# Kernel tuning notes

Hardware: AMD Instinct MI355X
Metric: run time of the kernel (lower is better)

The kernel has to match this reference:

```python
import jax, jax.numpy as jnp
import numpy as np

H, HKV, D, HID = 16, 8, 128, 2048   # heads, kv heads, head_dim, hidden
TOTAL, NSEG = 2048, 4               # packed tokens, number of sequences
SEG = TOTAL // NSEG
EPS = 1e-6


def setup_inputs() -> dict:
    key = jax.random.key(0)
    ks = jax.random.split(key, 8)
    x = jax.random.normal(ks[0], (1, TOTAL, HID), jnp.float32)
    # RoPE tables, positions restart at each packed segment
    inv_freq = 1.0 / (10000.0 ** (jnp.arange(0, D, 2, dtype=jnp.float32) / D))
    pos = jnp.tile(jnp.arange(SEG, dtype=jnp.float32), NSEG)  # [TOTAL]
    ang = pos[:, None] * inv_freq[None, :]                    # [TOTAL, D/2]
    emb = jnp.concatenate([ang, ang], axis=-1)                # [TOTAL, D]
    cos, sin = jnp.cos(emb), jnp.sin(emb)
    std = 0.02
    Wq = jax.random.normal(ks[1], (H * D, HID), jnp.float32) * std
    Wk = jax.random.normal(ks[2], (HKV * D, HID), jnp.float32) * std
    Wv = jax.random.normal(ks[3], (HKV * D, HID), jnp.float32) * std
    Wo = jax.random.normal(ks[4], (HID, H * D), jnp.float32) * std
    q_norm_w = jnp.ones((D,), jnp.float32)
    k_norm_w = jnp.ones((D,), jnp.float32)
    cu_seqlens = (jnp.arange(NSEG + 1, dtype=jnp.int32) * SEG)
    return {
        'x': x, 'cos': cos, 'sin': sin,
        'cu_seqlens': cu_seqlens, 'max_seqlen': SEG,
        'Wq': Wq, 'Wk': Wk, 'Wv': Wv, 'Wo': Wo,
        'q_norm_w': q_norm_w, 'k_norm_w': k_norm_w,
    }


def _rms(x, w):
    xf = x.astype(jnp.float32)
    var = jnp.mean(xf * xf, axis=-1, keepdims=True)
    return (w * xf * jax.lax.rsqrt(var + EPS)).astype(x.dtype)


def _rotate_half(x):
    x1, x2 = jnp.split(x, 2, axis=-1)
    return jnp.concatenate([-x2, x1], axis=-1)


def reference(x, cos, sin, cu_seqlens, max_seqlen, Wq, Wk, Wv, Wo, q_norm_w, k_norm_w):
    total = x.shape[1]
    xt = x[0]                                   # [total, HID]
    q = (xt @ Wq.T).reshape(total, H, D)
    k = (xt @ Wk.T).reshape(total, HKV, D)
    v = (xt @ Wv.T).reshape(total, HKV, D)
    q = _rms(q, q_norm_w)
    k = _rms(k, k_norm_w)
    c = cos[:, None, :]                          # [total, 1, D]
    s = sin[:, None, :]
    q = q * c + _rotate_half(q) * s
    k = k * c + _rotate_half(k) * s
    # GQA: repeat kv heads
    n_rep = H // HKV
    k = jnp.repeat(k, n_rep, axis=1)             # [total, H, D]
    v = jnp.repeat(v, n_rep, axis=1)
    # varlen causal mask (block-diagonal causal from cu_seqlens)
    idx = jnp.arange(total)
    seg = jnp.searchsorted(cu_seqlens[1:], idx, side='right')
    mask = (seg[:, None] == seg[None, :]) & (idx[:, None] >= idx[None, :])
    scale = 1.0 / jnp.sqrt(jnp.float32(D))
    scores = jnp.einsum('qhd,khd->hqk', q, k) * scale
    scores = jnp.where(mask[None, :, :], scores, -jnp.inf)
    probs = jax.nn.softmax(scores, axis=-1)
    out = jnp.einsum('hqk,khd->qhd', probs, v).reshape(1, total, H * D)
    return out @ Wo.T
```

## Files before the change

kernel.cpp:

```cpp
#include <hip/hip_runtime.h>
#include <hip/hip_bf16.h>
#include <stdint.h>

#define TOTAL 2048
#define NSEG  4
#define SEG   512
#define NH    16
#define NKV   8
#define DH    128
#define HID   2048
#define QKV_N 4096

typedef __attribute__((ext_vector_type(8))) __bf16 bf16x8;
typedef __attribute__((ext_vector_type(8))) unsigned short u16x8;
typedef __attribute__((ext_vector_type(4))) float f32x4;

__device__ __forceinline__ unsigned short f2bf(float f) {
  unsigned int u = __float_as_uint(f);
  u += 0x7fffu + ((u >> 16) & 1u);
  return (unsigned short)(u >> 16);
}

__device__ __forceinline__ void gll16(const void* g, void* l) {
  __builtin_amdgcn_global_load_lds(
      (const __attribute__((address_space(1))) void*)(uintptr_t)g,
      (__attribute__((address_space(3))) void*)(uint32_t)(uintptr_t)l,
      16, 0, 0);
}
__device__ __forceinline__ void cfence() { asm volatile("" ::: "memory"); }

__global__ __launch_bounds__(256) void cvt_all(const float* __restrict__ x,
                                               const float* __restrict__ wq,
                                               const float* __restrict__ wk,
                                               const float* __restrict__ wv,
                                               const float* __restrict__ wo,
                                               unsigned short* __restrict__ xb,
                                               unsigned short* __restrict__ wqkvb,
                                               unsigned short* __restrict__ wob) {
  const int N0 = 1048576, N1 = 1048576, N2 = 524288, N3 = 524288;
  int i = blockIdx.x * 256 + threadIdx.x;
  #pragma unroll
  for (int it = 0; it < 4; ++it, i += 1048576) {
    const float* src; unsigned short* dst; int j = i;
    if (j < N0)              { src = x;  dst = xb; }
    else if ((j -= N0) < N1) { src = wq; dst = wqkvb; }
    else if ((j -= N1) < N2) { src = wk; dst = wqkvb + 4194304; }
    else if ((j -= N2) < N3) { src = wv; dst = wqkvb + 6291456; }
    else                     { j -= N3; src = wo; dst = wob; }
    float4 v = reinterpret_cast<const float4*>(src)[j];
    ushort4 o;
    o.x = f2bf(v.x); o.y = f2bf(v.y); o.z = f2bf(v.z); o.w = f2bf(v.w);
    reinterpret_cast<ushort4*>(dst)[j] = o;
  }
}

template<int BM>
__global__ __launch_bounds__(BM == 128 ? 256 : 128)
void gemm_bt(const unsigned short* __restrict__ A,
             const unsigned short* __restrict__ B,
             float* __restrict__ C, int M, int N, int K) {
  constexpr int NW  = (BM == 128) ? 4 : 2;
  constexpr int APW = (BM / 8) / NW;
  constexpr int BPW = 16 / NW;
  __shared__ unsigned short As[2][BM * 64];
  __shared__ unsigned short Bs[2][128 * 64];
  const int t    = threadIdx.x;
  const int lane = t & 63;
  const int w    = t >> 6;
  const int wr   = (BM == 128) ? (w >> 1) * 64 : 0;
  const int wc   = (BM == 128) ? (w & 1) * 64 : w * 64;
  const long row0 = (long)blockIdx.y * BM;
  const long col0 = (long)blockIdx.x * 128;

  const int lrow  = lane >> 3;
  const int gslot = (lane & 7) ^ (lrow & 7);
  const unsigned short* gA[APW]; int lA[APW];
  const unsigned short* gB[BPW]; int lB[BPW];
  #pragma unroll
  for (int j = 0; j < APW; ++j) {
    const int c = w * APW + j;
    gA[j] = A + (row0 + c * 8 + lrow) * (long)K + gslot * 8;
    lA[j] = c * 512;
  }
  #pragma unroll
  for (int j = 0; j < BPW; ++j) {
    const int c = w * BPW + j;
    gB[j] = B + (col0 + c * 8 + lrow) * (long)K + gslot * 8;
    lB[j] = c * 512;
  }

  const int fr = lane & 15;
  const int l4 = lane >> 4;

  f32x4 acc[4][4];
  #pragma unroll
  for (int m = 0; m < 4; ++m)
    #pragma unroll
    for (int n = 0; n < 4; ++n) acc[m][n] = (f32x4){0.f, 0.f, 0.f, 0.f};

  #pragma unroll
  for (int j = 0; j < APW; ++j) gll16(gA[j], &As[0][lA[j]]);
  #pragma unroll
  for (int j = 0; j < BPW; ++j) gll16(gB[j], &Bs[0][lB[j]]);
  asm volatile("s_waitcnt vmcnt(0)" ::: "memory");
  __builtin_amdgcn_s_barrier();
  cfence();

  int cur = 0;
  for (int k0 = 0; k0 < K; k0 += 64) {
    if (k0 + 64 < K) {
      #pragma unroll
      for (int j = 0; j < APW; ++j) gll16(gA[j] + k0 + 64, &As[cur ^ 1][lA[j]]);
      #pragma unroll
      for (int j = 0; j < BPW; ++j) gll16(gB[j] + k0 + 64, &Bs[cur ^ 1][lB[j]]);
      if constexpr (BM == 128) asm volatile("s_waitcnt vmcnt(8)" ::: "memory");
      else                     asm volatile("s_waitcnt vmcnt(12)" ::: "memory");
    } else {
      asm volatile("s_waitcnt vmcnt(0)" ::: "memory");
    }
    __builtin_amdgcn_s_barrier();
    cfence();

    #pragma unroll
    for (int kk = 0; kk < 2; ++kk) {
      bf16x8 af[4], bfv[4];
      #pragma unroll
      for (int m = 0; m < 4; ++m) {
        const int ra = wr + m * 16 + fr;
        af[m] = *reinterpret_cast<const bf16x8*>(
            &As[cur][ra * 64 + (((kk * 4 + l4) ^ (ra & 7)) * 8)]);
      }
      #pragma unroll
      for (int n = 0; n < 4; ++n) {
        const int rb = wc + n * 16 + fr;
        bfv[n] = *reinterpret_cast<const bf16x8*>(
            &Bs[cur][rb * 64 + (((kk * 4 + l4) ^ (rb & 7)) * 8)]);
      }
      #pragma unroll
      for (int m = 0; m < 4; ++m)
        #pragma unroll
        for (int n = 0; n < 4; ++n)
          acc[m][n] = __builtin_amdgcn_mfma_f32_16x16x32_bf16(af[m], bfv[n], acc[m][n], 0, 0, 0);
    }

    cfence();
    __builtin_amdgcn_s_barrier();
    cfence();
    cur ^= 1;
  }

  const int crow = (lane >> 4) * 4;
  const int ccol = lane & 15;
  #pragma unroll
  for (int m = 0; m < 4; ++m)
    #pragma unroll
    for (int n = 0; n < 4; ++n)
      #pragma unroll
      for (int r = 0; r < 4; ++r)
        C[(row0 + wr + m * 16 + crow + r) * (long)N + col0 + wc + n * 16 + ccol] =
            acc[m][n][r];
}

__global__ __launch_bounds__(256) void norm_rope(const float* __restrict__ Cqkv,
                                                 const float* __restrict__ cosb,
                                                 const float* __restrict__ sinb,
                                                 const float* __restrict__ qw,
                                                 const float* __restrict__ kw,
                                                 unsigned short* __restrict__ qb2,
                                                 unsigned short* __restrict__ ktb) {
  const int lane = threadIdx.x & 63;
  const int t  = blockIdx.x * 4 + (threadIdx.x >> 6);
  const int hs = blockIdx.y;

  const float* row = Cqkv + (size_t)t * QKV_N + hs * DH;
  float a = row[lane];
  float b = row[lane + 64];

  float ss = a * a + b * b;
  #pragma unroll
  for (int off = 32; off; off >>= 1) ss += __shfl_xor(ss, off, 64);
  float r = rsqrtf(ss * (1.0f / 128.0f) + 1e-6f);
  const float* wgt = (hs < 16) ? qw : kw;
  a = a * r * wgt[lane];
  b = b * r * wgt[lane + 64];
  float c0 = cosb[t * DH + lane],      c1 = cosb[t * DH + lane + 64];
  float s0 = sinb[t * DH + lane],      s1 = sinb[t * DH + lane + 64];
  float o0 = a * c0 - b * s0;
  float o1 = b * c1 + a * s1;

  unsigned short* dst = (hs < 16)
      ? qb2 + ((size_t)hs * TOTAL + t) * DH
      : ktb + ((size_t)(hs - 16) * TOTAL + t) * DH;
  dst[lane]      = f2bf(o0);
  dst[lane + 64] = f2bf(o1);
}

__global__ __launch_bounds__(256) void vt_kernel(const float* __restrict__ Cqkv,
                                                 unsigned short* __restrict__ vtb) {
  __shared__ unsigned short tile[64][132];
  const int tid = threadIdx.x;
  const int t0  = blockIdx.x * 64;
  const int hkv = blockIdx.y;
  const float* src = Cqkv + (size_t)t0 * QKV_N + (NH + NKV) * DH + hkv * DH;
  #pragma unroll
  for (int it = 0; it < 8; ++it) {
    const int i   = it * 256 + tid;
    const int row = i >> 5;
    const int c4  = i & 31;
    float4 v = *reinterpret_cast<const float4*>(src + (size_t)row * QKV_N + c4 * 4);
    ushort4 o;
    o.x = f2bf(v.x); o.y = f2bf(v.y); o.z = f2bf(v.z); o.w = f2bf(v.w);
    *reinterpret_cast<ushort4*>(&tile[row][c4 * 4]) = o;
  }
  __syncthreads();
  #pragma unroll
  for (int it = 0; it < 4; ++it) {
    const int i  = it * 256 + tid;
    const int d  = i >> 3;
    const int tc = i & 7;
    u16x8 o;
    #pragma unroll
    for (int j = 0; j < 8; ++j) o[j] = tile[tc * 8 + j][d];
    *reinterpret_cast<u16x8*>(vtb + ((size_t)hkv * DH + d) * TOTAL + t0 + tc * 8) = o;
  }
}

__global__ __launch_bounds__(256) void attn_mfma(const unsigned short* __restrict__ qb2,
                                                 const unsigned short* __restrict__ ktb,
                                                 const unsigned short* __restrict__ vtb,
                                                 unsigned short* __restrict__ aob) {
  __shared__ unsigned short Ks[2][64 * 128];
  __shared__ unsigned short Vt[2][128 * 64];
  __shared__ unsigned short ps[4][16][72];

  const int tid  = threadIdx.x;
  const int lane = tid & 63;
  const int w    = tid >> 6;
  const int b    = blockIdx.x;
  const int qt   = 7 - (b & 7);
  const int h    = (b >> 3) & 15;
  const int seg  = b >> 7;
  const int hkv  = h >> 1;
  const int q0   = seg * SEG + qt * 64;
  const int l15  = lane & 15;
  const int l4   = lane >> 4;

  const unsigned short* qptr = qb2 + ((size_t)h * TOTAL + q0 + w * 16 + l15) * DH + l4 * 8;
  bf16x8 aq[4];
  #pragma unroll
  for (int ks = 0; ks < 4; ++ks)
    aq[ks] = *reinterpret_cast<const bf16x8*>(qptr + ks * 32);

  const unsigned short* kbase = ktb + (size_t)hkv * TOTAL * DH;
  const unsigned short* vbase = vtb + (size_t)hkv * DH * TOTAL;

  int ksrc[4], vsrc[4], ldst[4];
  #pragma unroll
  for (int j = 0; j < 4; ++j) {
    const int cc = w * 4 + j;
    const int kr = cc * 4 + (lane >> 4);
    ksrc[j] = kr * DH + (((lane & 15) ^ (kr & 7)) * 8);
    const int vd = cc * 8 + (lane >> 3);
    vsrc[j] = vd * TOTAL + (((lane & 7) ^ (vd & 7)) * 8);
    ldst[j] = cc * 512;
  }

  f32x4 acc[8];
  #pragma unroll
  for (int n = 0; n < 8; ++n) acc[n] = (f32x4){0.f, 0.f, 0.f, 0.f};
  float m_r[4] = {-1e30f, -1e30f, -1e30f, -1e30f};
  float l_r[4] = {0.f, 0.f, 0.f, 0.f};

  const float scale = 0.08838834764831845f;
  const int kvS = seg * SEG;

  #pragma unroll
  for (int j = 0; j < 4; ++j) {
    gll16(kbase + (size_t)kvS * DH + ksrc[j], &Ks[0][ldst[j]]);
    gll16(vbase + kvS + vsrc[j], &Vt[0][ldst[j]]);
  }
  asm volatile("s_waitcnt vmcnt(0)" ::: "memory");
  __builtin_amdgcn_s_barrier();
  cfence();

  int cur = 0;
  for (int kt = 0; kt <= qt; ++kt) {
    const int kv0 = kvS + kt * 64;
    if (kt < qt) {
      #pragma unroll
      for (int j = 0; j < 4; ++j) {
        gll16(kbase + (size_t)(kv0 + 64) * DH + ksrc[j], &Ks[cur ^ 1][ldst[j]]);
        gll16(vbase + (kv0 + 64) + vsrc[j], &Vt[cur ^ 1][ldst[j]]);
      }
      asm volatile("s_waitcnt vmcnt(8)" ::: "memory");
    } else {
      asm volatile("s_waitcnt vmcnt(0)" ::: "memory");
    }
    __builtin_amdgcn_s_barrier();
    cfence();

    const bool diag = (kt == qt);

    f32x4 sv[4];
    #pragma unroll
    for (int c = 0; c < 4; ++c) {
      if (diag && c * 16 > w * 16 + 15) {
        sv[c] = (f32x4){-1e30f, -1e30f, -1e30f, -1e30f};
      } else {
        f32x4 s = (f32x4){0.f, 0.f, 0.f, 0.f};
        const int kr = c * 16 + l15;
        #pragma unroll
        for (int ks = 0; ks < 4; ++ks) {
          const int byte = (kr << 8) + (((ks * 32 + l4 * 8) * 2) ^ ((kr & 7) << 4));
          bf16x8 bk = *reinterpret_cast<const bf16x8*>((const char*)Ks[cur] + byte);
          s = __builtin_amdgcn_mfma_f32_16x16x32_bf16(aq[ks], bk, s, 0, 0, 0);
        }
        sv[c] = s;
      }
    }

    float p[4][4];
    #pragma unroll
    for (int r = 0; r < 4; ++r) {
      const int qq = w * 16 + l4 * 4 + r;
      float mx = -1e30f;
      #pragma unroll
      for (int c = 0; c < 4; ++c) {
        float s = sv[c][r] * scale;
        if (diag) {
          const int kk = c * 16 + l15;
          if (kk > qq) s = -1e30f;
        }
        p[c][r] = s;
        mx = fmaxf(mx, s);
      }
      #pragma unroll
      for (int off = 1; off < 16; off <<= 1) mx = fmaxf(mx, __shfl_xor(mx, off));
      const float nm = fmaxf(m_r[r], mx);
      const float f  = __expf(m_r[r] - nm);
      m_r[r] = nm;
      float ls = 0.f;
      #pragma unroll
      for (int c = 0; c < 4; ++c) { p[c][r] = __expf(p[c][r] - nm); ls += p[c][r]; }
      #pragma unroll
      for (int off = 1; off < 16; off <<= 1) ls += __shfl_xor(ls, off);
      l_r[r] = l_r[r] * f + ls;
      #pragma unroll
      for (int n = 0; n < 8; ++n) acc[n][r] *= f;
    }

    #pragma unroll
    for (int c = 0; c < 4; ++c)
      #pragma unroll
      for (int r = 0; r < 4; ++r)
        ps[w][l4 * 4 + r][c * 16 + l15] = f2bf(p[c][r]);

    #pragma unroll
    for (int ks2 = 0; ks2 < 2; ++ks2) {
      if (diag && ks2 * 32 > w * 16 + 15) continue;
      bf16x8 pa = *reinterpret_cast<const bf16x8*>(&ps[w][l15][ks2 * 32 + l4 * 8]);
      #pragma unroll
      for (int n = 0; n < 8; ++n) {
        const int d = n * 16 + l15;
        const int byte = (d << 7) + (((ks2 * 32 + l4 * 8) * 2) ^ ((d & 7) << 4));
        bf16x8 bv = *reinterpret_cast<const bf16x8*>((const char*)Vt[cur] + byte);
        acc[n] = __builtin_amdgcn_mfma_f32_16x16x32_bf16(pa, bv, acc[n], 0, 0, 0);
      }
    }

    cfence();
    __builtin_amdgcn_s_barrier();
    cfence();
    cur ^= 1;
  }

  #pragma unroll
  for (int r = 0; r < 4; ++r) {
    const float inv = 1.0f / l_r[r];
    unsigned short* orow = aob + ((size_t)(q0 + w * 16 + l4 * 4 + r) * NH + h) * DH;
    #pragma unroll
    for (int n = 0; n < 8; ++n)
      orow[n * 16 + l15] = f2bf(acc[n][r] * inv);
  }
}

extern "C" void kernel_launch(void* const* d_in, const int* in_sizes, int n_in,
                              void* d_out, int out_size, void* d_ws, size_t ws_size,
                              hipStream_t stream) {
  const float* x    = (const float*)d_in[0];
  const float* cosb = (const float*)d_in[1];
  const float* sinb = (const float*)d_in[2];
  const float* Wq   = (const float*)d_in[5];
  const float* Wk   = (const float*)d_in[6];
  const float* Wv   = (const float*)d_in[7];
  const float* Wo   = (const float*)d_in[8];
  const float* qw   = (const float*)d_in[9];
  const float* kw   = (const float*)d_in[10];
  float* out = (float*)d_out;

  char* ws = (char*)d_ws;
  unsigned short* xb    = (unsigned short*)(ws + 0);
  unsigned short* Wqkvb = (unsigned short*)(ws + (8u  << 20));
  unsigned short* Wob   = (unsigned short*)(ws + (24u << 20));
  float*          Cqkv  = (float*)         (ws + (32u << 20));
  unsigned short* qb2   = (unsigned short*)(ws + (64u << 20));
  unsigned short* ktb   = (unsigned short*)(ws + (72u << 20));
  unsigned short* vtb   = (unsigned short*)(ws + (76u << 20));
  unsigned short* aob   = (unsigned short*)(ws + (80u << 20));

  cvt_all<<<4096, 256, 0, stream>>>(x, Wq, Wk, Wv, Wo, xb, Wqkvb, Wob);

  {
    dim3 g(QKV_N / 128, TOTAL / 128);
    gemm_bt<128><<<g, 256, 0, stream>>>(xb, Wqkvb, Cqkv, TOTAL, QKV_N, HID);
  }

  {
    dim3 g(TOTAL / 4, 24);
    norm_rope<<<g, 256, 0, stream>>>(Cqkv, cosb, sinb, qw, kw, qb2, ktb);
  }
  {
    dim3 g(TOTAL / 64, NKV);
    vt_kernel<<<g, 256, 0, stream>>>(Cqkv, vtb);
  }

  attn_mfma<<<NSEG * NH * 8, 256, 0, stream>>>(qb2, ktb, vtb, aob);

  {
    dim3 g(HID / 128, TOTAL / 64);
    gemm_bt<64><<<g, 128, 0, stream>>>(aob, Wob, out, TOTAL, HID, HID);
  }
}
```

Measured before the change: 122.7 us.

## Fuse QK RMSNorm, RoPE and V transpose into QKV GEMM epilogue

Adds a dedicated QKV GEMM kernel whose epilogue computes per-head RMSNorm via cross-wave shared reductions, applies RoPE, and writes bf16 Q/K or transposed V directly. This removes the fp32 QKV intermediate round trip through global memory and two separate kernel launches. The epilogue reuses the 69KB shared buffer for a padded tile, which raises LDS use and may lower occupancy.

```diff
diff --git a/kernel.cpp b/kernel.cpp
--- a/kernel.cpp
+++ b/kernel.cpp
@@ -51,6 +51,176 @@
     ushort4 o;
     o.x = f2bf(v.x); o.y = f2bf(v.y); o.z = f2bf(v.z); o.w = f2bf(v.w);
     reinterpret_cast<ushort4*>(dst)[j] = o;
+  }
+}
+
+__global__ __launch_bounds__(256)
+void gemm_qkv(const unsigned short* __restrict__ A,
+              const unsigned short* __restrict__ B,
+              const float* __restrict__ cosb,
+              const float* __restrict__ sinb,
+              const float* __restrict__ qw,
+              const float* __restrict__ kw,
+              unsigned short* __restrict__ qb2,
+              unsigned short* __restrict__ ktb,
+              unsigned short* __restrict__ vtb) {
+  __shared__ char smem[69120] __attribute__((aligned(16)));
+  unsigned short* As0 = (unsigned short*)smem;
+  unsigned short* Bs0 = (unsigned short*)(smem + 32768);
+  const int K = HID;
+  const int t    = threadIdx.x;
+  const int lane = t & 63;
+  const int w    = t >> 6;
+  const int wr   = (w >> 1) * 64;
+  const int wc   = (w & 1) * 64;
+  const long row0 = (long)blockIdx.y * 128;
+  const long col0 = (long)blockIdx.x * 128;
+
+  const int lrow  = lane >> 3;
+  const int gslot = (lane & 7) ^ (lrow & 7);
+  const unsigned short* gA[4]; const unsigned short* gB[4]; int loff[4];
+  #pragma unroll
+  for (int j = 0; j < 4; ++j) {
+    const int c = w * 4 + j;
+    gA[j] = A + (row0 + c * 8 + lrow) * (long)K + gslot * 8;
+    gB[j] = B + (col0 + c * 8 + lrow) * (long)K + gslot * 8;
+    loff[j] = c * 512;
+  }
+
+  const int fr = lane & 15;
+  const int l4 = lane >> 4;
+
+  f32x4 acc[4][4];
+  #pragma unroll
+  for (int m = 0; m < 4; ++m)
+    #pragma unroll
+    for (int n = 0; n < 4; ++n) acc[m][n] = (f32x4){0.f, 0.f, 0.f, 0.f};
+
+  #pragma unroll
+  for (int j = 0; j < 4; ++j) { gll16(gA[j], As0 + loff[j]); gll16(gB[j], Bs0 + loff[j]); }
+  asm volatile("s_waitcnt vmcnt(0)" ::: "memory");
+  __builtin_amdgcn_s_barrier();
+  cfence();
+
+  int cur = 0;
+  for (int k0 = 0; k0 < K; k0 += 64) {
+    if (k0 + 64 < K) {
+      #pragma unroll
+      for (int j = 0; j < 4; ++j) {
+        gll16(gA[j] + k0 + 64, As0 + (cur ^ 1) * 8192 + loff[j]);
+        gll16(gB[j] + k0 + 64, Bs0 + (cur ^ 1) * 8192 + loff[j]);
+      }
+      asm volatile("s_waitcnt vmcnt(8)" ::: "memory");
+    } else {
+      asm volatile("s_waitcnt vmcnt(0)" ::: "memory");
+    }
+    __builtin_amdgcn_s_barrier();
+    cfence();
+
+    #pragma unroll
+    for (int kk = 0; kk < 2; ++kk) {
+      bf16x8 af[4], bfv[4];
+      #pragma unroll
+      for (int m = 0; m < 4; ++m) {
+        const int ra = wr + m * 16 + fr;
+        af[m] = *reinterpret_cast<const bf16x8*>(
+            As0 + cur * 8192 + ra * 64 + (((kk * 4 + l4) ^ (ra & 7)) * 8));
+      }
+      #pragma unroll
+      for (int n = 0; n < 4; ++n) {
+        const int rb = wc + n * 16 + fr;
+        bfv[n] = *reinterpret_cast<const bf16x8*>(
+            Bs0 + cur * 8192 + rb * 64 + (((kk * 4 + l4) ^ (rb & 7)) * 8));
+      }
+      #pragma unroll
+      for (int m = 0; m < 4; ++m)
+        #pragma unroll
+        for (int n = 0; n < 4; ++n)
+          acc[m][n] = __builtin_amdgcn_mfma_f32_16x16x32_bf16(af[m], bfv[n], acc[m][n], 0, 0, 0);
+    }
+
+    cfence();
+    __builtin_amdgcn_s_barrier();
+    cfence();
+    cur ^= 1;
+  }
+
+  float* td  = (float*)smem;
+  float* ssq = (float*)(smem + 68096);
+  const int hs   = blockIdx.x;
+  const int crow = (lane >> 4) * 4;
+  const int ccol = lane & 15;
+  const bool isv = (hs >= 24);
+
+  float rms[4][4];
+  #pragma unroll
+  for (int m = 0; m < 4; ++m)
+    #pragma unroll
+    for (int r = 0; r < 4; ++r) {
+      float ss = 0.f;
+      #pragma unroll
+      for (int n = 0; n < 4; ++n) ss += acc[m][n][r] * acc[m][n][r];
+      #pragma unroll
+      for (int off = 1; off < 16; off <<= 1) ss += __shfl_xor(ss, off);
+      rms[m][r] = ss;
+    }
+  if ((lane & 15) == 0) {
+    #pragma unroll
+    for (int m = 0; m < 4; ++m)
+      #pragma unroll
+      for (int r = 0; r < 4; ++r)
+        ssq[(w >> 1) * 128 + (w & 1) * 64 + m * 16 + crow + r] = rms[m][r];
+  }
+  __syncthreads();
+  #pragma unroll
+  for (int m = 0; m < 4; ++m)
+    #pragma unroll
+    for (int r = 0; r < 4; ++r) {
+      const int row64 = m * 16 + crow + r;
+      const float tot = ssq[(w >> 1) * 128 + row64] + ssq[(w >> 1) * 128 + 64 + row64];
+      rms[m][r] = rsqrtf(tot * (1.0f / 128.0f) + 1e-6f);
+    }
+
+  const float* wgt = (hs < 16) ? qw : kw;
+  #pragma unroll
+  for (int n = 0; n < 4; ++n) {
+    const int col = wc + n * 16 + ccol;
+    const float wv_ = isv ? 1.f : wgt[col];
+    #pragma unroll
+    for (int m = 0; m < 4; ++m)
+      #pragma unroll
+      for (int r = 0; r < 4; ++r) {
+        float v = acc[m][n][r];
+        if (!isv) v *= rms[m][r] * wv_;
+        td[(wr + m * 16 + crow + r) * 133 + col] = v;
+      }
+  }
+  __syncthreads();
+
+  if (!isv) {
+    unsigned short* base = (hs < 16)
+        ? qb2 + (size_t)hs * TOTAL * DH
+        : ktb + (size_t)(hs - 16) * TOTAL * DH;
+    for (int i = t; i < 128 * 64; i += 256) {
+      const int row = i >> 6, d = i & 63;
+      const float a = td[row * 133 + d];
+      const float b = td[row * 133 + d + 64];
+      const long tg = row0 + row;
+      const float c0 = cosb[tg * DH + d],      c1 = cosb[tg * DH + d + 64];
+      const float s0 = sinb[tg * DH + d],      s1 = sinb[tg * DH + d + 64];
+      unsigned short* dst = base + (size_t)tg * DH;
+      dst[d]      = f2bf(a * c0 - b * s0);
+      dst[d + 64] = f2bf(b * c1 + a * s1);
+    }
+  } else {
+    unsigned short* base = vtb + (size_t)(hs - 24) * DH * TOTAL;
+    for (int i = t; i < 128 * 16; i += 256) {
+      const int d = i >> 4, tb = i & 15;
+      u16x8 o;
+      #pragma unroll
+      for (int j = 0; j < 8; ++j) o[j] = f2bf(td[(tb * 8 + j) * 133 + d]);
+      *reinterpret_cast<u16x8*>(base + (size_t)d * TOTAL + row0 + tb * 8) = o;
+    }
   }
 }
 
@@ -161,70 +331,6 @@
             acc[m][n][r];
 }
 
-__global__ __launch_bounds__(256) void norm_rope(const float* __restrict__ Cqkv,
-                                                 const float* __restrict__ cosb,
-                                                 const float* __restrict__ sinb,
-                                                 const float* __restrict__ qw,
-                                                 const float* __restrict__ kw,
-                                                 unsigned short* __restrict__ qb2,
-                                                 unsigned short* __restrict__ ktb) {
-  const int lane = threadIdx.x & 63;
-  const int t  = blockIdx.x * 4 + (threadIdx.x >> 6);
-  const int hs = blockIdx.y;
-
-  const float* row = Cqkv + (size_t)t * QKV_N + hs * DH;
-  float a = row[lane];
-  float b = row[lane + 64];
-
-  float ss = a * a + b * b;
-  #pragma unroll
-  for (int off = 32; off; off >>= 1) ss += __shfl_xor(ss, off, 64);
-  float r = rsqrtf(ss * (1.0f / 128.0f) + 1e-6f);
-  const float* wgt = (hs < 16) ? qw : kw;
-  a = a * r * wgt[lane];
-  b = b * r * wgt[lane + 64];
-  float c0 = cosb[t * DH + lane],      c1 = cosb[t * DH + lane + 64];
-  float s0 = sinb[t * DH + lane],      s1 = sinb[t * DH + lane + 64];
-  float o0 = a * c0 - b * s0;
-  float o1 = b * c1 + a * s1;
-
-  unsigned short* dst = (hs < 16)
-      ? qb2 + ((size_t)hs * TOTAL + t) * DH
-      : ktb + ((size_t)(hs - 16) * TOTAL + t) * DH;
-  dst[lane]      = f2bf(o0);
-  dst[lane + 64] = f2bf(o1);
-}
-
-__global__ __launch_bounds__(256) void vt_kernel(const float* __restrict__ Cqkv,
-                                                 unsigned short* __restrict__ vtb) {
-  __shared__ unsigned short tile[64][132];
-  const int tid = threadIdx.x;
-  const int t0  = blockIdx.x * 64;
-  const int hkv = blockIdx.y;
-  const float* src = Cqkv + (size_t)t0 * QKV_N + (NH + NKV) * DH + hkv * DH;
-  #pragma unroll
-  for (int it = 0; it < 8; ++it) {
-    const int i   = it * 256 + tid;
-    const int row = i >> 5;
-    const int c4  = i & 31;
-    float4 v = *reinterpret_cast<const float4*>(src + (size_t)row * QKV_N + c4 * 4);
-    ushort4 o;
-    o.x = f2bf(v.x); o.y = f2bf(v.y); o.z = f2bf(v.z); o.w = f2bf(v.w);
-    *reinterpret_cast<ushort4*>(&tile[row][c4 * 4]) = o;
-  }
-  __syncthreads();
-  #pragma unroll
-  for (int it = 0; it < 4; ++it) {
-    const int i  = it * 256 + tid;
-    const int d  = i >> 3;
-    const int tc = i & 7;
-    u16x8 o;
-    #pragma unroll
-    for (int j = 0; j < 8; ++j) o[j] = tile[tc * 8 + j][d];
-    *reinterpret_cast<u16x8*>(vtb + ((size_t)hkv * DH + d) * TOTAL + t0 + tc * 8) = o;
-  }
-}
-
 __global__ __launch_bounds__(256) void attn_mfma(const unsigned short* __restrict__ qb2,
                                                  const unsigned short* __restrict__ ktb,
                                                  const unsigned short* __restrict__ vtb,
@@ -402,7 +508,6 @@
   unsigned short* xb    = (unsigned short*)(ws + 0);
   unsigned short* Wqkvb = (unsigned short*)(ws + (8u  << 20));
   unsigned short* Wob   = (unsigned short*)(ws + (24u << 20));
-  float*          Cqkv  = (float*)         (ws + (32u << 20));
   unsigned short* qb2   = (unsigned short*)(ws + (64u << 20));
   unsigned short* ktb   = (unsigned short*)(ws + (72u << 20));
   unsigned short* vtb   = (unsigned short*)(ws + (76u << 20));
@@ -412,16 +517,7 @@
 
   {
     dim3 g(QKV_N / 128, TOTAL / 128);
-    gemm_bt<128><<<g, 256, 0, stream>>>(xb, Wqkvb, Cqkv, TOTAL, QKV_N, HID);
-  }
-
-  {
-    dim3 g(TOTAL / 4, 24);
-    norm_rope<<<g, 256, 0, stream>>>(Cqkv, cosb, sinb, qw, kw, qb2, ktb);
-  }
-  {
-    dim3 g(TOTAL / 64, NKV);
-    vt_kernel<<<g, 256, 0, stream>>>(Cqkv, vtb);
+    gemm_qkv<<<g, 256, 0, stream>>>(xb, Wqkvb, cosb, sinb, qw, kw, qb2, ktb, vtb);
   }
 
   attn_mfma<<<NSEG * NH * 8, 256, 0, stream>>>(qb2, ktb, vtb, aob);
```

After: 115.5 us. 1.06x faster.
